# Kernel tuning notes

Hardware: AMD Instinct MI355X
Metric: run time of the kernel (lower is better)

Reference implementation:

```python
import jax, jax.numpy as jnp
import numpy as np

B, T, J, D, H = 64, 240, 22, 128, 8


def setup_inputs() -> dict:
    key = jax.random.key(0)
    ks = jax.random.split(key, 6)
    x = jax.random.normal(ks[0], (B, T, J, D), dtype=jnp.float32)
    adjacency = jax.random.randint(ks[1], (J, J), 0, 2, dtype=jnp.int32)
    # self-loops so no softmax row is fully masked (matches sane graph usage)
    adjacency = adjacency.at[jnp.arange(J), jnp.arange(J)].set(1)
    in_proj_w = jax.random.normal(ks[2], (3 * D, D), dtype=jnp.float32) * 0.05
    in_proj_b = jax.random.normal(ks[3], (3 * D,), dtype=jnp.float32) * 0.02
    out_w = jax.random.normal(ks[4], (D, D), dtype=jnp.float32) * 0.05
    out_b = jax.random.normal(ks[5], (D,), dtype=jnp.float32) * 0.02
    return {"x": x, "adjacency": adjacency, "in_proj_w": in_proj_w,
            "in_proj_b": in_proj_b, "out_w": out_w, "out_b": out_b}


def reference(x, adjacency, in_proj_w, in_proj_b, out_w, out_b):
    b, t, j, d = x.shape
    hd = d // H
    n = b * t
    x_bt = x.reshape(n, j, d)
    # combined QKV projection (nn.MultiheadAttention in_proj)
    qkv = x_bt @ in_proj_w.T + in_proj_b            # [n, j, 3d]
    q, k, v = jnp.split(qkv, 3, axis=-1)
    split_heads = lambda a: a.reshape(n, j, H, hd).transpose(0, 2, 1, 3)  # [n,H,j,hd]
    q, k, v = split_heads(q), split_heads(k), split_heads(v)
    scores = jnp.einsum('nhqd,nhkd->nhqk', q, k) / np.sqrt(hd).astype(np.float32)
    mask = adjacency <= 0                            # True = disallowed (bool attn_mask)
    scores = jnp.where(mask[None, None], -jnp.inf, scores)
    attn = jax.nn.softmax(scores, axis=-1)
    y = jnp.einsum('nhqk,nhkd->nhqd', attn, v)       # [n,H,j,hd]
    y = y.transpose(0, 2, 1, 3).reshape(n, j, d)
    y = y @ out_w.T + out_b                          # out_proj
    return y.reshape(b, t, j, d)
```

## Files before the change

kernel.cpp:

```cpp
#include <hip/hip_runtime.h>

typedef _Float16 f16;
typedef __fp16 h16x2 __attribute__((ext_vector_type(2)));
typedef _Float16 f16x4 __attribute__((ext_vector_type(4)));
typedef _Float16 f16x8 __attribute__((ext_vector_type(8)));
typedef float f32x4 __attribute__((ext_vector_type(4)));

#define N_ROWS   337920
#define RG       44
#define NGROUPS  7680
#define QKV_ROWB  512
#define QKV_BYTES (48 * QKV_ROWB)
#define VT_OFF    QKV_BYTES
#define LDS_BYTES (QKV_BYTES + 128 * 64 * 2)
#define WQKV_F16  49152
#define WOUT_F16  16384
#define MASK_OFF  ((WQKV_F16 + WOUT_F16) * 2)
#define WS_NEEDED (MASK_OFF + 4096)
#define SCQ 0.3606737602222409f

__device__ __forceinline__ uint32_t swz(int row, int bytecol) {
  return (uint32_t)((row * QKV_ROWB + bytecol) ^ ((row & 7) << 4));
}
__device__ __forceinline__ uint32_t vswz(int d, int col) {
  return (uint32_t)(VT_OFF + ((d * 128 + col * 2) ^ ((d & 15) << 3)));
}
__device__ __forceinline__ f16x8 pack8z(float4 a, float4 b) {
  h16x2 p0 = __builtin_amdgcn_cvt_pkrtz(a.x, a.y);
  h16x2 p1 = __builtin_amdgcn_cvt_pkrtz(a.z, a.w);
  h16x2 p2 = __builtin_amdgcn_cvt_pkrtz(b.x, b.y);
  h16x2 p3 = __builtin_amdgcn_cvt_pkrtz(b.z, b.w);
  f16x8 r;
  r[0]=p0[0]; r[1]=p0[1]; r[2]=p1[0]; r[3]=p1[1];
  r[4]=p2[0]; r[5]=p2[1]; r[6]=p3[0]; r[7]=p3[1];
  return r;
}
__device__ __forceinline__ f16x4 pack4z(float a, float b, float c, float d) {
  h16x2 p0 = __builtin_amdgcn_cvt_pkrtz(a, b);
  h16x2 p1 = __builtin_amdgcn_cvt_pkrtz(c, d);
  f16x4 r;
  r[0]=p0[0]; r[1]=p0[1]; r[2]=p1[0]; r[3]=p1[1];
  return r;
}

__global__ void prep(const float* __restrict__ wqkv, const float* __restrict__ wout,
                     const int* __restrict__ adj, char* __restrict__ ws) {
  f16* w16 = (f16*)ws;
  int b = blockIdx.x;
  if (b < 64) {
    int i4 = (b * 256 + threadIdx.x) * 4;
    const float* src = (i4 < WQKV_F16) ? (wqkv + i4) : (wout + (i4 - WQKV_F16));
    float4 v = *(const float4*)src;
    f16x4 h;
    h[0]=(f16)v.x; h[1]=(f16)v.y; h[2]=(f16)v.z; h[3]=(f16)v.w;
    *(f16x4*)(w16 + i4) = h;
  } else {
    int t = threadIdx.x;
    int qt = t >> 7, jt = (t >> 6) & 1, l = t & 63;
    int g = l >> 4, r16 = l & 15;
    f32x4 m;
    #pragma unroll
    for (int r = 0; r < 4; r++) {
      int q = qt * 16 + r16, j = jt * 16 + 4 * g + r;
      float v = -1e30f;
      if (j < 22) v = (q >= 22 || adj[q * 22 + j] > 0) ? 0.0f : -1e30f;
      m[r] = v;
    }
    *(f32x4*)(ws + MASK_OFF + t * 16) = m;
  }
}

template <int F16M>
__global__ __launch_bounds__(256, 2)
void mga_fused(const float* __restrict__ x, const int* __restrict__ adj,
               const float* __restrict__ bqkv, const float* __restrict__ bout,
               const char* __restrict__ ws, const float* __restrict__ wqkv32,
               const float* __restrict__ wout32,
               float* __restrict__ out) {
  __shared__ __align__(16) char smem[LDS_BYTES];
  const int tid = threadIdx.x;
  const int wv = tid >> 6;
  const int l = tid & 63;
  const int g = l >> 4;
  const int r16 = l & 15;
  const long g0 = (long)blockIdx.x * RG;
  const f16* w16 = (const f16*)ws;
  const f16* w16o = w16 + WQKV_F16;

  {
    int d = 16 * wv + 64 * ((l >> 5) & 1) + (l & 15);
    int c0 = ((l >> 4) & 1) ? 54 : 22;
    #pragma unroll
    for (int i = 0; i < 5; i++)
      *(int*)(smem + vswz(d, c0 + 2 * i)) = 0;
  }

  f16x8 xf[3][4];
  #pragma unroll
  for (int mt = 0; mt < 3; mt++) {
    long rowg = g0 + mt * 16 + r16;
    if (rowg > (long)N_ROWS - 1) rowg = N_ROWS - 1;
    const float* xp = x + rowg * 128 + g * 8;
    #pragma unroll
    for (int ks = 0; ks < 4; ks++)
      xf[mt][ks] = pack8z(*(const float4*)(xp + ks * 32),
                          *(const float4*)(xp + ks * 32 + 4));
  }

  f16x8 wcur[4], wnxt[4];
  {
    int wrow = wv * 16 + r16;
    #pragma unroll
    for (int ks = 0; ks < 4; ks++) {
      int off = wrow * 128 + ks * 32 + g * 8;
      if (F16M) wcur[ks] = *(const f16x8*)(w16 + off);
      else      wcur[ks] = pack8z(*(const float4*)(wqkv32 + off),
                                  *(const float4*)(wqkv32 + off + 4));
    }
  }
  #pragma unroll 1
  for (int i = 0; i < 6; i++) {
    int nt = wv + 4 * i;
    if (i < 5) {
      int wrow = (nt + 4) * 16 + r16;
      #pragma unroll
      for (int ks = 0; ks < 4; ks++) {
        int off = wrow * 128 + ks * 32 + g * 8;
        if (F16M) wnxt[ks] = *(const f16x8*)(w16 + off);
        else      wnxt[ks] = pack8z(*(const float4*)(wqkv32 + off),
                                    *(const float4*)(wqkv32 + off + 4));
      }
    }
    if (nt < 16) {
      f32x4 bb = *(const f32x4*)(bqkv + nt * 16 + 4 * g);
      f32x4 acc[3] = {bb, bb, bb};
      #pragma unroll
      for (int ks = 0; ks < 4; ks++) {
        acc[0] = __builtin_amdgcn_mfma_f32_16x16x32_f16(wcur[ks], xf[0][ks], acc[0], 0,0,0);
        acc[1] = __builtin_amdgcn_mfma_f32_16x16x32_f16(wcur[ks], xf[1][ks], acc[1], 0,0,0);
        acc[2] = __builtin_amdgcn_mfma_f32_16x16x32_f16(wcur[ks], xf[2][ks], acc[2], 0,0,0);
      }
      float sc = (nt < 8) ? SCQ : 1.0f;
      int col = nt * 16 + 4 * g;
      #pragma unroll
      for (int mt = 0; mt < 3; mt++) {
        f16x4 h4 = pack4z(acc[mt][0] * sc, acc[mt][1] * sc,
                          acc[mt][2] * sc, acc[mt][3] * sc);
        *(f16x4*)(smem + swz(mt * 16 + r16, col * 2)) = h4;
      }
    } else {
      float bvs = bqkv[nt * 16 + r16];
      f32x4 bb = {bvs, bvs, bvs, bvs};
      f32x4 acc[3] = {bb, bb, bb};
      #pragma unroll
      for (int ks = 0; ks < 4; ks++) {
        acc[0] = __builtin_amdgcn_mfma_f32_16x16x32_f16(xf[0][ks], wcur[ks], acc[0], 0,0,0);
        acc[1] = __builtin_amdgcn_mfma_f32_16x16x32_f16(xf[1][ks], wcur[ks], acc[1], 0,0,0);
        acc[2] = __builtin_amdgcn_mfma_f32_16x16x32_f16(xf[2][ks], wcur[ks], acc[2], 0,0,0);
      }
      int d = (nt - 16) * 16 + r16;
      #pragma unroll
      for (int mt = 0; mt < 3; mt++) {
        #pragma unroll
        for (int p = 0; p < 2; p++) {
          int rowl = mt * 16 + 4 * g + 2 * p;
          int t = rowl >= 22;
          int col = rowl + 10 * t;
          h16x2 v2 = __builtin_amdgcn_cvt_pkrtz(acc[mt][2*p], acc[mt][2*p+1]);
          *(h16x2*)(smem + vswz(d, col)) = v2;
        }
      }
    }
    #pragma unroll
    for (int ks = 0; ks < 4; ks++) wcur[ks] = wnxt[ks];
  }

  f32x4 mq[2][2];
  if (F16M) {
    #pragma unroll
    for (int qt = 0; qt < 2; qt++)
      #pragma unroll
      for (int jt = 0; jt < 2; jt++)
        mq[qt][jt] = *(const f32x4*)(ws + MASK_OFF + ((qt * 2 + jt) * 64 + l) * 16);
  } else {
    #pragma unroll
    for (int qt = 0; qt < 2; qt++)
      #pragma unroll
      for (int jt = 0; jt < 2; jt++)
        #pragma unroll
        for (int r = 0; r < 4; r++) {
          int q = qt * 16 + r16, j = jt * 16 + 4 * g + r;
          float m = -1e30f;
          if (j < 22) m = (q >= 22 || adj[q * 22 + j] > 0) ? 0.0f : -1e30f;
          mq[qt][jt][r] = m;
        }
  }

  f16x8 wf3a[4];
  #pragma unroll
  for (int ks = 0; ks < 4; ks++) {
    int off = (2 * wv * 16 + r16) * 128 + ks * 32 + g * 8;
    if (F16M) wf3a[ks] = *(const f16x8*)(w16o + off);
    else      wf3a[ks] = pack8z(*(const float4*)(wout32 + off),
                                *(const float4*)(wout32 + off + 4));
  }

  __syncthreads();

  {
    const int t = wv >> 1;
    const int rbase = 22 * t;
    const int hbase = 4 * (wv & 1);
    const int rowk0 = rbase + r16;
    int rk1 = rbase + 16 + r16; if (rk1 > 47) rk1 = 47;
    const int rowk1 = rk1;
    #pragma unroll 1
    for (int hi = 0; hi < 4; hi++) {
      int h = hbase + hi;
      f16x4 kf0 = *(const f16x4*)(smem + swz(rowk0, (128 + h * 16 + 4 * g) * 2));
      f16x4 kf1 = *(const f16x4*)(smem + swz(rowk1, (128 + h * 16 + 4 * g) * 2));
      f16x4 vf0 = *(const f16x4*)(smem + vswz(h * 16 + r16, t * 32 + 4 * g));
      f16x4 vf1 = *(const f16x4*)(smem + vswz(h * 16 + r16, t * 32 + 16 + 4 * g));
      #pragma unroll
      for (int qt = 0; qt < 2; qt++) {
        int rowq = qt ? rowk1 : rowk0;
        f16x4 qf = *(const f16x4*)(smem + swz(rowq, (h * 16 + 4 * g) * 2));
        f32x4 z = {0.f, 0.f, 0.f, 0.f};
        f32x4 s0 = __builtin_amdgcn_mfma_f32_16x16x16f16(kf0, qf, z, 0, 0, 0);
        f32x4 s1 = __builtin_amdgcn_mfma_f32_16x16x16f16(kf1, qf, z, 0, 0, 0);
        float p[8];
        #pragma unroll
        for (int r = 0; r < 4; r++) {
          p[r]     = __builtin_exp2f(s0[r] + mq[qt][0][r]);
          p[4 + r] = __builtin_exp2f(s1[r] + mq[qt][1][r]);
        }
        float sum = ((p[0] + p[1]) + (p[2] + p[3])) + ((p[4] + p[5]) + (p[6] + p[7]));
        sum += __shfl_xor(sum, 16, 64);
        sum += __shfl_xor(sum, 32, 64);
        f16x4 pb0 = pack4z(p[0], p[1], p[2], p[3]);
        f16x4 pb1 = pack4z(p[4], p[5], p[6], p[7]);
        f32x4 ya = __builtin_amdgcn_mfma_f32_16x16x16f16(vf0, pb0, z, 0, 0, 0);
        ya = __builtin_amdgcn_mfma_f32_16x16x16f16(vf1, pb1, ya, 0, 0, 0);
        float inv = __builtin_amdgcn_rcpf(sum);
        int q = qt * 16 + r16;
        if (q < 22) {
          f16x4 yh = pack4z(ya[0] * inv, ya[1] * inv, ya[2] * inv, ya[3] * inv);
          *(f16x4*)(smem + swz(rbase + q, (h * 16 + 4 * g) * 2)) = yh;
        }
      }
    }
  }
  __syncthreads();

  f16x8 wf3b[4];
  #pragma unroll
  for (int ks = 0; ks < 4; ks++) {
    int off = ((2 * wv + 1) * 16 + r16) * 128 + ks * 32 + g * 8;
    if (F16M) wf3b[ks] = *(const f16x8*)(w16o + off);
    else      wf3b[ks] = pack8z(*(const float4*)(wout32 + off),
                                *(const float4*)(wout32 + off + 4));
  }
  f32x4 bva = *(const f32x4*)(bout + 2 * wv * 16 + 4 * g);
  f32x4 bvb = *(const f32x4*)(bout + (2 * wv + 1) * 16 + 4 * g);
  #pragma unroll 1
  for (int mt = 0; mt < 3; mt++) {
    f16x8 af[4];
    #pragma unroll
    for (int ks = 0; ks < 4; ks++)
      af[ks] = *(const f16x8*)(smem + swz(mt * 16 + r16, (ks * 32 + g * 8) * 2));
    int rowl = mt * 16 + r16;
    f32x4 acc0 = bva, acc1 = bvb;
    #pragma unroll
    for (int ks = 0; ks < 4; ks++) {
      acc0 = __builtin_amdgcn_mfma_f32_16x16x32_f16(wf3a[ks], af[ks], acc0, 0, 0, 0);
      acc1 = __builtin_amdgcn_mfma_f32_16x16x32_f16(wf3b[ks], af[ks], acc1, 0, 0, 0);
    }
    if (rowl < RG) {
      float4 oa, ob;
      oa.x = acc0[0]; oa.y = acc0[1]; oa.z = acc0[2]; oa.w = acc0[3];
      ob.x = acc1[0]; ob.y = acc1[1]; ob.z = acc1[2]; ob.w = acc1[3];
      *(float4*)(out + (g0 + rowl) * 128 + 2 * wv * 16 + 4 * g) = oa;
      *(float4*)(out + (g0 + rowl) * 128 + (2 * wv + 1) * 16 + 4 * g) = ob;
    }
  }
}

extern "C" void kernel_launch(void* const* d_in, const int* in_sizes, int n_in,
                              void* d_out, int out_size, void* d_ws, size_t ws_size,
                              hipStream_t stream) {
  const float* x    = (const float*)d_in[0];
  const int*   adj  = (const int*)d_in[1];
  const float* wqkv = (const float*)d_in[2];
  const float* bqkv = (const float*)d_in[3];
  const float* wout = (const float*)d_in[4];
  const float* bout = (const float*)d_in[5];
  float* o = (float*)d_out;

  int f16m = (d_ws != nullptr && ws_size >= (size_t)WS_NEEDED) ? 1 : 0;
  if (f16m) {
    prep<<<dim3(65), dim3(256), 0, stream>>>(wqkv, wout, adj, (char*)d_ws);
    mga_fused<1><<<dim3(NGROUPS), dim3(256), 0, stream>>>(
        x, adj, bqkv, bout, (const char*)d_ws, wqkv, wout, o);
  } else {
    mga_fused<0><<<dim3(NGROUPS), dim3(256), 0, stream>>>(
        x, adj, bqkv, bout, (const char*)d_ws, wqkv, wout, o);
  }
}
```

Baseline: 222.3 us.

## Compute V projection in-register per head to drop LDS V buffer and raise occupancy

The V projection is no longer computed in the shared QKV loop and staged transposed in LDS. Instead, each wave reloads its time-step's x rows and computes V for each head directly in registers right before the attention MFMA. This removes the 16KB V transpose region from LDS and its zero-init, and launch bounds are raised to five blocks per SM. In exchange, x rows are loaded twice and more register pressure falls on the attention loop, which could cause spills at the higher occupancy target.

```diff
diff --git a/kernel.cpp b/kernel.cpp
--- a/kernel.cpp
+++ b/kernel.cpp
@@ -10,9 +10,7 @@
 #define RG       44
 #define NGROUPS  7680
 #define QKV_ROWB  512
-#define QKV_BYTES (48 * QKV_ROWB)
-#define VT_OFF    QKV_BYTES
-#define LDS_BYTES (QKV_BYTES + 128 * 64 * 2)
+#define LDS_BYTES (48 * QKV_ROWB)
 #define WQKV_F16  49152
 #define WOUT_F16  16384
 #define MASK_OFF  ((WQKV_F16 + WOUT_F16) * 2)
@@ -21,9 +19,6 @@
 
 __device__ __forceinline__ uint32_t swz(int row, int bytecol) {
   return (uint32_t)((row * QKV_ROWB + bytecol) ^ ((row & 7) << 4));
-}
-__device__ __forceinline__ uint32_t vswz(int d, int col) {
-  return (uint32_t)(VT_OFF + ((d * 128 + col * 2) ^ ((d & 15) << 3)));
 }
 __device__ __forceinline__ f16x8 pack8z(float4 a, float4 b) {
   h16x2 p0 = __builtin_amdgcn_cvt_pkrtz(a.x, a.y);
@@ -71,7 +66,7 @@
 }
 
 template <int F16M>
-__global__ __launch_bounds__(256, 2)
+__global__ __launch_bounds__(256, 5)
 void mga_fused(const float* __restrict__ x, const int* __restrict__ adj,
                const float* __restrict__ bqkv, const float* __restrict__ bout,
                const char* __restrict__ ws, const float* __restrict__ wqkv32,
@@ -86,14 +81,8 @@
   const long g0 = (long)blockIdx.x * RG;
   const f16* w16 = (const f16*)ws;
   const f16* w16o = w16 + WQKV_F16;
-
-  {
-    int d = 16 * wv + 64 * ((l >> 5) & 1) + (l & 15);
-    int c0 = ((l >> 4) & 1) ? 54 : 22;
-    #pragma unroll
-    for (int i = 0; i < 5; i++)
-      *(int*)(smem + vswz(d, c0 + 2 * i)) = 0;
-  }
+  const int t = wv >> 1;
+  const int hbase = 4 * (wv & 1);
 
   f16x8 xf[3][4];
   #pragma unroll
@@ -106,6 +95,18 @@
       xf[mt][ks] = pack8z(*(const float4*)(xp + ks * 32),
                           *(const float4*)(xp + ks * 32 + 4));
   }
+  f16x8 xfv[2][4];
+  {
+    const long tb = g0 + 22 * t;
+    int rv1 = 16 + r16; if (rv1 > 21) rv1 = 21;
+    const float* xv0 = x + (tb + r16) * 128 + g * 8;
+    const float* xv1 = x + (tb + rv1) * 128 + g * 8;
+    #pragma unroll
+    for (int ks = 0; ks < 4; ks++) {
+      xfv[0][ks] = pack8z(*(const float4*)(xv0 + ks * 32), *(const float4*)(xv0 + ks * 32 + 4));
+      xfv[1][ks] = pack8z(*(const float4*)(xv1 + ks * 32), *(const float4*)(xv1 + ks * 32 + 4));
+    }
+  }
 
   f16x8 wcur[4], wnxt[4];
   {
@@ -119,9 +120,9 @@
     }
   }
   #pragma unroll 1
-  for (int i = 0; i < 6; i++) {
+  for (int i = 0; i < 4; i++) {
     int nt = wv + 4 * i;
-    if (i < 5) {
+    if (i < 3) {
       int wrow = (nt + 4) * 16 + r16;
       #pragma unroll
       for (int ks = 0; ks < 4; ks++) {
@@ -131,45 +132,21 @@
                                     *(const float4*)(wqkv32 + off + 4));
       }
     }
-    if (nt < 16) {
-      f32x4 bb = *(const f32x4*)(bqkv + nt * 16 + 4 * g);
-      f32x4 acc[3] = {bb, bb, bb};
-      #pragma unroll
-      for (int ks = 0; ks < 4; ks++) {
-        acc[0] = __builtin_amdgcn_mfma_f32_16x16x32_f16(wcur[ks], xf[0][ks], acc[0], 0,0,0);
-        acc[1] = __builtin_amdgcn_mfma_f32_16x16x32_f16(wcur[ks], xf[1][ks], acc[1], 0,0,0);
-        acc[2] = __builtin_amdgcn_mfma_f32_16x16x32_f16(wcur[ks], xf[2][ks], acc[2], 0,0,0);
-      }
-      float sc = (nt < 8) ? SCQ : 1.0f;
-      int col = nt * 16 + 4 * g;
-      #pragma unroll
-      for (int mt = 0; mt < 3; mt++) {
-        f16x4 h4 = pack4z(acc[mt][0] * sc, acc[mt][1] * sc,
-                          acc[mt][2] * sc, acc[mt][3] * sc);
-        *(f16x4*)(smem + swz(mt * 16 + r16, col * 2)) = h4;
-      }
-    } else {
-      float bvs = bqkv[nt * 16 + r16];
-      f32x4 bb = {bvs, bvs, bvs, bvs};
-      f32x4 acc[3] = {bb, bb, bb};
-      #pragma unroll
-      for (int ks = 0; ks < 4; ks++) {
-        acc[0] = __builtin_amdgcn_mfma_f32_16x16x32_f16(xf[0][ks], wcur[ks], acc[0], 0,0,0);
-        acc[1] = __builtin_amdgcn_mfma_f32_16x16x32_f16(xf[1][ks], wcur[ks], acc[1], 0,0,0);
-        acc[2] = __builtin_amdgcn_mfma_f32_16x16x32_f16(xf[2][ks], wcur[ks], acc[2], 0,0,0);
-      }
-      int d = (nt - 16) * 16 + r16;
-      #pragma unroll
-      for (int mt = 0; mt < 3; mt++) {
-        #pragma unroll
-        for (int p = 0; p < 2; p++) {
-          int rowl = mt * 16 + 4 * g + 2 * p;
-          int t = rowl >= 22;
-          int col = rowl + 10 * t;
-          h16x2 v2 = __builtin_amdgcn_cvt_pkrtz(acc[mt][2*p], acc[mt][2*p+1]);
-          *(h16x2*)(smem + vswz(d, col)) = v2;
-        }
-      }
+    f32x4 bb = *(const f32x4*)(bqkv + nt * 16 + 4 * g);
+    f32x4 acc[3] = {bb, bb, bb};
+    #pragma unroll
+    for (int ks = 0; ks < 4; ks++) {
+      acc[0] = __builtin_amdgcn_mfma_f32_16x16x32_f16(wcur[ks], xf[0][ks], acc[0], 0,0,0);
+      acc[1] = __builtin_amdgcn_mfma_f32_16x16x32_f16(wcur[ks], xf[1][ks], acc[1], 0,0,0);
+      acc[2] = __builtin_amdgcn_mfma_f32_16x16x32_f16(wcur[ks], xf[2][ks], acc[2], 0,0,0);
+    }
+    float sc = (nt < 8) ? SCQ : 1.0f;
+    int col = nt * 16 + 4 * g;
+    #pragma unroll
+    for (int mt = 0; mt < 3; mt++) {
+      f16x4 h4 = pack4z(acc[mt][0] * sc, acc[mt][1] * sc,
+                        acc[mt][2] * sc, acc[mt][3] * sc);
+      *(f16x4*)(smem + swz(mt * 16 + r16, col * 2)) = h4;
     }
     #pragma unroll
     for (int ks = 0; ks < 4; ks++) wcur[ks] = wnxt[ks];
@@ -196,31 +173,37 @@
         }
   }
 
-  f16x8 wf3a[4];
-  #pragma unroll
-  for (int ks = 0; ks < 4; ks++) {
-    int off = (2 * wv * 16 + r16) * 128 + ks * 32 + g * 8;
-    if (F16M) wf3a[ks] = *(const f16x8*)(w16o + off);
-    else      wf3a[ks] = pack8z(*(const float4*)(wout32 + off),
-                                *(const float4*)(wout32 + off + 4));
-  }
-
   __syncthreads();
 
   {
-    const int t = wv >> 1;
     const int rbase = 22 * t;
-    const int hbase = 4 * (wv & 1);
     const int rowk0 = rbase + r16;
     int rk1 = rbase + 16 + r16; if (rk1 > 47) rk1 = 47;
     const int rowk1 = rk1;
     #pragma unroll 1
     for (int hi = 0; hi < 4; hi++) {
       int h = hbase + hi;
+      f16x8 wvf[4];
+      #pragma unroll
+      for (int ks = 0; ks < 4; ks++) {
+        int off = (256 + h * 16 + r16) * 128 + ks * 32 + g * 8;
+        if (F16M) wvf[ks] = *(const f16x8*)(w16 + off);
+        else      wvf[ks] = pack8z(*(const float4*)(wqkv32 + off),
+                                   *(const float4*)(wqkv32 + off + 4));
+      }
+      float bvs = bqkv[256 + h * 16 + r16];
+      f32x4 bbv = {bvs, bvs, bvs, bvs};
+      f32x4 aV0 = bbv, aV1 = bbv;
+      #pragma unroll
+      for (int ks = 0; ks < 4; ks++) {
+        aV0 = __builtin_amdgcn_mfma_f32_16x16x32_f16(xfv[0][ks], wvf[ks], aV0, 0,0,0);
+        aV1 = __builtin_amdgcn_mfma_f32_16x16x32_f16(xfv[1][ks], wvf[ks], aV1, 0,0,0);
+      }
+      f16x4 vf0 = pack4z(aV0[0], aV0[1], aV0[2], aV0[3]);
+      f16x4 vf1 = pack4z(aV1[0], aV1[1], aV1[2], aV1[3]);
+
       f16x4 kf0 = *(const f16x4*)(smem + swz(rowk0, (128 + h * 16 + 4 * g) * 2));
       f16x4 kf1 = *(const f16x4*)(smem + swz(rowk1, (128 + h * 16 + 4 * g) * 2));
-      f16x4 vf0 = *(const f16x4*)(smem + vswz(h * 16 + r16, t * 32 + 4 * g));
-      f16x4 vf1 = *(const f16x4*)(smem + vswz(h * 16 + r16, t * 32 + 16 + 4 * g));
       #pragma unroll
       for (int qt = 0; qt < 2; qt++) {
         int rowq = qt ? rowk1 : rowk0;
@@ -252,13 +235,18 @@
   }
   __syncthreads();
 
-  f16x8 wf3b[4];
+  f16x8 wf3a[4], wf3b[4];
   #pragma unroll
   for (int ks = 0; ks < 4; ks++) {
-    int off = ((2 * wv + 1) * 16 + r16) * 128 + ks * 32 + g * 8;
-    if (F16M) wf3b[ks] = *(const f16x8*)(w16o + off);
-    else      wf3b[ks] = pack8z(*(const float4*)(wout32 + off),
-                                *(const float4*)(wout32 + off + 4));
+    int offa = (2 * wv * 16 + r16) * 128 + ks * 32 + g * 8;
+    int offb = ((2 * wv + 1) * 16 + r16) * 128 + ks * 32 + g * 8;
+    if (F16M) {
+      wf3a[ks] = *(const f16x8*)(w16o + offa);
+      wf3b[ks] = *(const f16x8*)(w16o + offb);
+    } else {
+      wf3a[ks] = pack8z(*(const float4*)(wout32 + offa), *(const float4*)(wout32 + offa + 4));
+      wf3b[ks] = pack8z(*(const float4*)(wout32 + offb), *(const float4*)(wout32 + offb + 4));
+    }
   }
   f32x4 bva = *(const f32x4*)(bout + 2 * wv * 16 + 4 * g);
   f32x4 bvb = *(const f32x4*)(bout + (2 * wv + 1) * 16 + 4 * g);
```

After: 452.2 us. +103.4%, slower.
